# Optimization experiments

Measured on AMD Instinct MI355X. Metric: run time of the kernel, lower is better.

The kernel has to match this reference:

```python
import jax, jax.numpy as jnp
import numpy as np

G, T, D_IN, D_OUT = 8, 8192, 1024, 1024
# fixed uneven per-expert token counts summing to T (variable-size groups)
_COUNTS = np.array([512, 1536, 1024, 1024, 768, 1280, 896, 1152], dtype=np.int32)
assert _COUNTS.sum() == T


def setup_inputs() -> dict:
    key = jax.random.key(0)
    k1, k2 = jax.random.split(key)
    hidden_states = jax.random.normal(k1, (T, D_IN), dtype=jnp.float32)
    # kaiming_uniform_(a=sqrt(5)) on [G, in, out] -> bound = sqrt(3/ (fan_in)) with gain sqrt(1/3)
    bound = 1.0 / np.sqrt(D_IN)
    weight = jax.random.uniform(k2, (G, D_IN, D_OUT), dtype=jnp.float32, minval=-bound, maxval=bound)
    tokens_per_expert = jnp.asarray(_COUNTS)
    return {"hidden_states": hidden_states, "weight": weight, "tokens_per_expert": tokens_per_expert}


def reference(hidden_states, weight, tokens_per_expert):
    # grouped GEMM: token t in group g (per contiguous split by tokens_per_expert)
    # gets out[t] = hidden_states[t] @ weight[g]
    T_ = hidden_states.shape[0]
    G_ = weight.shape[0]
    offsets = jnp.cumsum(tokens_per_expert)  # [G] end offsets of each group
    expert_id = jnp.searchsorted(offsets, jnp.arange(T_), side="right")  # [T]
    out = jnp.zeros((T_, weight.shape[2]), dtype=hidden_states.dtype)
    for g in range(G_):  # small fixed expert count; masked accumulate keeps shapes static
        mask = (expert_id == g).astype(hidden_states.dtype)[:, None]
        out = out + mask * (hidden_states @ weight[g])
    return out
```

## Files before the change

kernel.cpp:

```cpp
#include <hip/hip_runtime.h>
#include <hip/hip_bf16.h>
#include <stdint.h>

typedef __attribute__((ext_vector_type(8))) short short8;
typedef __attribute__((ext_vector_type(4))) short short4s;
typedef __attribute__((ext_vector_type(4))) float f32x4;

constexpr int Tt = 8192, Kd = 1024, Nd = 1024, Gn = 8;
constexpr int BM = 128, BN = 256, BK = 64;
constexpr int NKT = Kd / BK;

static __device__ __forceinline__ short f2bf(float x) {
    __hip_bfloat16 b = __float2bfloat16(x);
    return *reinterpret_cast<short*>(&b);
}

__global__ __launch_bounds__(256)
void prep_kernel(const float* __restrict__ H, const float* __restrict__ W,
                 short* __restrict__ Hb, short* __restrict__ Wt)
{
    const int b = blockIdx.x, t = threadIdx.x;
    if (b < 2048) {
        const int g = b >> 8, r = b & 255;
        const int kb = (r >> 4) * 64, nb = (r & 15) * 64;
        const float* src = W + (size_t)g * Kd * Nd + (size_t)kb * Nd + nb;
        __shared__ float Ls[64 * 64];
#pragma unroll
        for (int i = 0; i < 4; ++i) {
            const int s = i * 256 + t;
            const int k = s >> 4, gc = s & 15;
            const f32x4 v = *(const f32x4*)(src + (size_t)k * Nd + ((gc ^ (k & 15)) << 2));
            *(f32x4*)&Ls[k * 64 + (gc << 2)] = v;
        }
        __syncthreads();
        short* dst = Wt + (size_t)g * Nd * Kd + (size_t)nb * Kd + kb;
#pragma unroll
        for (int i = 0; i < 2; ++i) {
            const int s = i * 256 + t;
            const int n = s >> 3, kc = s & 7;
            short8 v;
#pragma unroll
            for (int j = 0; j < 8; ++j) {
                const int k = kc * 8 + j;
                v[j] = f2bf(Ls[k * 64 + ((((n >> 2) ^ (k & 15)) << 2) | (n & 3))]);
            }
            *(short8*)(dst + (size_t)n * Kd + kc * 8) = v;
        }
    } else {
        const int hb = b - 2048;
#pragma unroll
        for (int i = 0; i < 8; ++i) {
            const size_t gidx = (size_t)i * 262144 + (size_t)hb * 256 + t;
            const f32x4 x = *(const f32x4*)(H + gidx * 4);
            short4s v;
#pragma unroll
            for (int j = 0; j < 4; ++j) v[j] = f2bf(x[j]);
            *(short4s*)(Hb + gidx * 4) = v;
        }
    }
}

__global__ __launch_bounds__(512, 2)
void gemm_bf16_kernel(const short* __restrict__ Hb, const short* __restrict__ Wt,
                      const int* __restrict__ counts, float* __restrict__ out)
{
    __shared__ __align__(16) short As[3][BM * BK];
    __shared__ __align__(16) short Bs[3][BN * BK];

    const int tid = threadIdx.x;
    const int bid = blockIdx.x;
    const int swz = (bid & 7) * 32 + (bid >> 3);
    const int mt = swz >> 2, nt = swz & 3;
    const int row0 = mt * BM, col0 = nt * BN;

    int g = 0;
    {
        int c = 0;
        for (int i = 0; i < Gn; ++i) { c += counts[i]; if (row0 >= c) g = i + 1; }
    }
    const short* __restrict__ Wg = Wt + (size_t)g * Nd * Kd;

    const int wid = tid >> 6, lane = tid & 63;
    const int wm = wid >> 2, wn = wid & 3;
    const int l15 = lane & 15, l4 = lane >> 4;

    f32x4 acc[4][4];
#pragma unroll
    for (int i = 0; i < 4; ++i)
#pragma unroll
        for (int j = 0; j < 4; ++j) acc[i][j] = (f32x4)0.0f;

    auto stage = [&](int kt, int buf) {
#pragma unroll
        for (int i = 0; i < 2; ++i) {
            const int q = i * 8 + wid;
            const int s = q * 64 + lane;
            const int row = s >> 3, gc = (s & 7) ^ (row & 7);
            const short* src = Hb + (size_t)(row0 + row) * Kd + kt * BK + gc * 8;
            __builtin_amdgcn_global_load_lds(
                (const __attribute__((address_space(1))) uint32_t*)src,
                (__attribute__((address_space(3))) uint32_t*)(&As[buf][q * 512]),
                16, 0, 0);
        }
#pragma unroll
        for (int i = 0; i < 4; ++i) {
            const int q = i * 8 + wid;
            const int s = q * 64 + lane;
            const int row = s >> 3, gc = (s & 7) ^ (row & 7);
            const short* src = Wg + (size_t)(col0 + row) * Kd + kt * BK + gc * 8;
            __builtin_amdgcn_global_load_lds(
                (const __attribute__((address_space(1))) uint32_t*)src,
                (__attribute__((address_space(3))) uint32_t*)(&Bs[buf][q * 512]),
                16, 0, 0);
        }
    };

    auto compute = [&](int buf) {
#pragma unroll
        for (int ks = 0; ks < 2; ++ks) {
            short8 af[4], bf[4];
#pragma unroll
            for (int mi = 0; mi < 4; ++mi) {
                const int m = wm * 64 + mi * 16 + l15;
                af[mi] = *(const short8*)&As[buf][m * 64 + (((ks * 4 + l4) ^ (m & 7)) << 3)];
            }
#pragma unroll
            for (int ni = 0; ni < 4; ++ni) {
                const int n = wn * 64 + ni * 16 + l15;
                bf[ni] = *(const short8*)&Bs[buf][n * 64 + (((ks * 4 + l4) ^ (n & 7)) << 3)];
            }
            __builtin_amdgcn_s_setprio(1);
#pragma unroll
            for (int mi = 0; mi < 4; ++mi)
#pragma unroll
                for (int ni = 0; ni < 4; ++ni)
                    acc[mi][ni] = __builtin_amdgcn_mfma_f32_16x16x32_bf16(
                        af[mi], bf[ni], acc[mi][ni], 0, 0, 0);
            __builtin_amdgcn_s_setprio(0);
        }
    };

    stage(0, 0);
    stage(1, 1);
    asm volatile("s_waitcnt vmcnt(6)" ::: "memory");
    __builtin_amdgcn_s_barrier();
    __builtin_amdgcn_sched_barrier(0);

    int b0 = 0, bs = 2;
    for (int kt = 0; kt < NKT; ++kt) {
        if (kt + 2 < NKT) stage(kt + 2, bs);
        compute(b0);
        if (kt + 1 < NKT) {
            if (kt + 2 < NKT) asm volatile("s_waitcnt vmcnt(6)" ::: "memory");
            else              asm volatile("s_waitcnt vmcnt(0)" ::: "memory");
            __builtin_amdgcn_s_barrier();
            __builtin_amdgcn_sched_barrier(0);
        }
        b0 = (b0 == 2) ? 0 : b0 + 1;
        bs = (bs == 2) ? 0 : bs + 1;
    }

#pragma unroll
    for (int mi = 0; mi < 4; ++mi) {
        const int rbase = row0 + wm * 64 + mi * 16 + l4 * 4;
#pragma unroll
        for (int ni = 0; ni < 4; ++ni) {
            const int c = col0 + wn * 64 + ni * 16 + l15;
#pragma unroll
            for (int r = 0; r < 4; ++r)
                out[(size_t)(rbase + r) * Nd + c] = acc[mi][ni][r];
        }
    }
}

__global__ __launch_bounds__(512, 2)
void gemm_f32_fallback(const float* __restrict__ H, const float* __restrict__ W,
                       const int* __restrict__ counts, float* __restrict__ out)
{
    __shared__ __align__(16) short As[2][BM * BK];
    __shared__ __align__(16) short Bs2[2][BN * BK];
    const int tid = threadIdx.x, bid = blockIdx.x;
    const int swz = (bid & 7) * 32 + (bid >> 3);
    const int mt = swz >> 2, nt = swz & 3;
    const int row0 = mt * BM, col0 = nt * BN;
    int g = 0; { int c = 0; for (int i = 0; i < Gn; ++i) { c += counts[i]; if (row0 >= c) g = i + 1; } }
    const float* __restrict__ Wg = W + (size_t)g * Kd * Nd;
    const int wid = tid >> 6, lane = tid & 63;
    const int wm = wid >> 2, wn = wid & 3;
    const int l15 = lane & 15, l4 = lane >> 4;
    const int ra = tid >> 2, ca = tid & 3;
    const int nb = tid & 255, kh = tid >> 8;
    f32x4 acc[4][4];
#pragma unroll
    for (int i = 0; i < 4; ++i)
#pragma unroll
        for (int j = 0; j < 4; ++j) acc[i][j] = (f32x4)0.0f;
    f32x4 av[4]; float bv[32];
    auto load_a = [&](int kt) {
        const float* p = H + (size_t)(row0 + ra) * Kd + kt * BK + ca * 16;
#pragma unroll
        for (int j = 0; j < 4; ++j) av[j] = *(const f32x4*)(p + j * 4);
    };
    auto load_b = [&](int kt) {
        const float* p = Wg + (size_t)(kt * BK + kh * 32) * Nd + col0 + nb;
#pragma unroll
        for (int j = 0; j < 32; ++j) bv[j] = p[(size_t)j * Nd];
    };
    auto write_a = [&](int buf) {
        short8 v0, v1;
#pragma unroll
        for (int j = 0; j < 4; ++j) {
            v0[j] = f2bf(av[0][j]); v0[4 + j] = f2bf(av[1][j]);
            v1[j] = f2bf(av[2][j]); v1[4 + j] = f2bf(av[3][j]);
        }
        const int s = ra & 7;
        *(short8*)&As[buf][ra * 64 + (((ca * 2) ^ s) << 3)] = v0;
        *(short8*)&As[buf][ra * 64 + (((ca * 2 + 1) ^ s) << 3)] = v1;
    };
    auto write_b = [&](int buf) {
        const int s = nb & 7;
#pragma unroll
        for (int c = 0; c < 4; ++c) {
            short8 v;
#pragma unroll
            for (int j = 0; j < 8; ++j) v[j] = f2bf(bv[c * 8 + j]);
            *(short8*)&Bs2[buf][nb * 64 + (((kh * 4 + c) ^ s) << 3)] = v;
        }
    };
    auto compute = [&](int buf) {
#pragma unroll
        for (int ks = 0; ks < 2; ++ks) {
            short8 af[4], bf[4];
#pragma unroll
            for (int mi = 0; mi < 4; ++mi) {
                const int m = wm * 64 + mi * 16 + l15;
                af[mi] = *(const short8*)&As[buf][m * 64 + (((ks * 4 + l4) ^ (m & 7)) << 3)];
            }
#pragma unroll
            for (int ni = 0; ni < 4; ++ni) {
                const int n = wn * 64 + ni * 16 + l15;
                bf[ni] = *(const short8*)&Bs2[buf][n * 64 + (((ks * 4 + l4) ^ (n & 7)) << 3)];
            }
#pragma unroll
            for (int mi = 0; mi < 4; ++mi)
#pragma unroll
                for (int ni = 0; ni < 4; ++ni)
                    acc[mi][ni] = __builtin_amdgcn_mfma_f32_16x16x32_bf16(
                        af[mi], bf[ni], acc[mi][ni], 0, 0, 0);
        }
    };
    load_a(0); load_b(0); write_a(0); write_b(0);
    __syncthreads();
    int buf = 0;
    for (int kt = 0; kt < NKT; ++kt) {
        const bool more = (kt + 1 < NKT);
        if (more) { load_a(kt + 1); load_b(kt + 1); }
        compute(buf);
        if (more) { write_a(buf ^ 1); write_b(buf ^ 1); }
        __syncthreads();
        buf ^= 1;
    }
#pragma unroll
    for (int mi = 0; mi < 4; ++mi) {
        const int rbase = row0 + wm * 64 + mi * 16 + l4 * 4;
#pragma unroll
        for (int ni = 0; ni < 4; ++ni) {
            const int c = col0 + wn * 64 + ni * 16 + l15;
#pragma unroll
            for (int r = 0; r < 4; ++r)
                out[(size_t)(rbase + r) * Nd + c] = acc[mi][ni][r];
        }
    }
}

extern "C" void kernel_launch(void* const* d_in, const int* in_sizes, int n_in,
                              void* d_out, int out_size, void* d_ws, size_t ws_size,
                              hipStream_t stream) {
    const float* H = (const float*)d_in[0];
    const float* W = (const float*)d_in[1];
    const int* counts = (const int*)d_in[2];
    float* out = (float*)d_out;
    const size_t need = (size_t)(Tt * Kd + Gn * Kd * Nd) * sizeof(short);
    if (ws_size >= need) {
        short* Hb = (short*)d_ws;
        short* Wt = Hb + (size_t)Tt * Kd;
        prep_kernel<<<3072, 256, 0, stream>>>(H, W, Hb, Wt);
        gemm_bf16_kernel<<<256, 512, 0, stream>>>(Hb, Wt, counts, out);
    } else {
        gemm_f32_fallback<<<256, 512, 0, stream>>>(H, W, counts, out);
    }
}
```

Before: 47.48 us.

## Split K-step into four interleaved load/read/MFMA phases with barriers

The per-K-tile work is restructured into four quadrant phases. Global-to-LDS staging of A and two halves of B is interleaved with LDS fragment reads and MFMA batches, separated by workgroup barriers, in the style of ping-pong scheduling. The goal is to overlap memory issue with matrix-core work and spread LDS traffic across the tile. The cost is many more barriers per iteration, which may add synchronisation stalls.

```diff
diff --git a/kernel.cpp b/kernel.cpp
--- a/kernel.cpp
+++ b/kernel.cpp
@@ -90,7 +90,7 @@
 #pragma unroll
         for (int j = 0; j < 4; ++j) acc[i][j] = (f32x4)0.0f;
 
-    auto stage = [&](int kt, int buf) {
+    auto stage_a = [&](int kt, int buf) {
 #pragma unroll
         for (int i = 0; i < 2; ++i) {
             const int q = i * 8 + wid;
@@ -102,9 +102,11 @@
                 (__attribute__((address_space(3))) uint32_t*)(&As[buf][q * 512]),
                 16, 0, 0);
         }
-#pragma unroll
-        for (int i = 0; i < 4; ++i) {
-            const int q = i * 8 + wid;
+    };
+    auto stage_b = [&](int kt, int buf, int half) {
+#pragma unroll
+        for (int i = 0; i < 2; ++i) {
+            const int q = (half * 2 + i) * 8 + wid;
             const int s = q * 64 + lane;
             const int row = s >> 3, gc = (s & 7) ^ (row & 7);
             const short* src = Wg + (size_t)(col0 + row) * Kd + kt * BK + gc * 8;
@@ -115,48 +117,100 @@
         }
     };
 
-    auto compute = [&](int buf) {
-#pragma unroll
-        for (int ks = 0; ks < 2; ++ks) {
-            short8 af[4], bf[4];
-#pragma unroll
-            for (int mi = 0; mi < 4; ++mi) {
-                const int m = wm * 64 + mi * 16 + l15;
-                af[mi] = *(const short8*)&As[buf][m * 64 + (((ks * 4 + l4) ^ (m & 7)) << 3)];
-            }
-#pragma unroll
-            for (int ni = 0; ni < 4; ++ni) {
-                const int n = wn * 64 + ni * 16 + l15;
-                bf[ni] = *(const short8*)&Bs[buf][n * 64 + (((ks * 4 + l4) ^ (n & 7)) << 3)];
-            }
-            __builtin_amdgcn_s_setprio(1);
-#pragma unroll
-            for (int mi = 0; mi < 4; ++mi)
-#pragma unroll
-                for (int ni = 0; ni < 4; ++ni)
-                    acc[mi][ni] = __builtin_amdgcn_mfma_f32_16x16x32_bf16(
-                        af[mi], bf[ni], acc[mi][ni], 0, 0, 0);
-            __builtin_amdgcn_s_setprio(0);
-        }
-    };
-
-    stage(0, 0);
-    stage(1, 1);
+    auto rd_a = [&](int buf, int mi, int ks) -> short8 {
+        const int m = wm * 64 + mi * 16 + l15;
+        return *(const short8*)&As[buf][m * 64 + (((ks * 4 + l4) ^ (m & 7)) << 3)];
+    };
+    auto rd_b = [&](int buf, int ni, int ks) -> short8 {
+        const int n = wn * 64 + ni * 16 + l15;
+        return *(const short8*)&Bs[buf][n * 64 + (((ks * 4 + l4) ^ (n & 7)) << 3)];
+    };
+
+    stage_a(0, 0); stage_b(0, 0, 0); stage_b(0, 0, 1);
+    stage_a(1, 1); stage_b(1, 1, 0); stage_b(1, 1, 1);
     asm volatile("s_waitcnt vmcnt(6)" ::: "memory");
     __builtin_amdgcn_s_barrier();
-    __builtin_amdgcn_sched_barrier(0);
-
-    int b0 = 0, bs = 2;
+
+    int bc = 0, bs = 2;
     for (int kt = 0; kt < NKT; ++kt) {
-        if (kt + 2 < NKT) stage(kt + 2, bs);
-        compute(b0);
-        if (kt + 1 < NKT) {
-            if (kt + 2 < NKT) asm volatile("s_waitcnt vmcnt(6)" ::: "memory");
-            else              asm volatile("s_waitcnt vmcnt(0)" ::: "memory");
-            __builtin_amdgcn_s_barrier();
-            __builtin_amdgcn_sched_barrier(0);
-        }
-        b0 = (b0 == 2) ? 0 : b0 + 1;
+        const bool pf = (kt + 2 < NKT);
+        short8 af0[2][2], af1[2][2], bf0[2][2], bf1[2][2];
+
+        if (pf) stage_a(kt + 2, bs);
+#pragma unroll
+        for (int i = 0; i < 2; ++i)
+#pragma unroll
+            for (int ks = 0; ks < 2; ++ks) { af0[i][ks] = rd_a(bc, i, ks); bf0[i][ks] = rd_b(bc, i, ks); }
+        __builtin_amdgcn_s_barrier();
+        asm volatile("s_waitcnt lgkmcnt(0)" ::: "memory");
+        __builtin_amdgcn_sched_barrier(0);
+        __builtin_amdgcn_s_setprio(1);
+#pragma unroll
+        for (int mi = 0; mi < 2; ++mi)
+#pragma unroll
+            for (int ni = 0; ni < 2; ++ni)
+#pragma unroll
+                for (int ks = 0; ks < 2; ++ks)
+                    acc[mi][ni] = __builtin_amdgcn_mfma_f32_16x16x32_bf16(
+                        af0[mi][ks], bf0[ni][ks], acc[mi][ni], 0, 0, 0);
+        __builtin_amdgcn_s_setprio(0);
+        __builtin_amdgcn_s_barrier();
+
+        if (pf) stage_b(kt + 2, bs, 0);
+#pragma unroll
+        for (int i = 0; i < 2; ++i)
+#pragma unroll
+            for (int ks = 0; ks < 2; ++ks) af1[i][ks] = rd_a(bc, 2 + i, ks);
+        __builtin_amdgcn_s_barrier();
+        asm volatile("s_waitcnt lgkmcnt(0)" ::: "memory");
+        __builtin_amdgcn_sched_barrier(0);
+        __builtin_amdgcn_s_setprio(1);
+#pragma unroll
+        for (int mi = 0; mi < 2; ++mi)
+#pragma unroll
+            for (int ni = 0; ni < 2; ++ni)
+#pragma unroll
+                for (int ks = 0; ks < 2; ++ks)
+                    acc[2 + mi][ni] = __builtin_amdgcn_mfma_f32_16x16x32_bf16(
+                        af1[mi][ks], bf0[ni][ks], acc[2 + mi][ni], 0, 0, 0);
+        __builtin_amdgcn_s_setprio(0);
+        __builtin_amdgcn_s_barrier();
+
+        if (pf) stage_b(kt + 2, bs, 1);
+#pragma unroll
+        for (int i = 0; i < 2; ++i)
+#pragma unroll
+            for (int ks = 0; ks < 2; ++ks) bf1[i][ks] = rd_b(bc, 2 + i, ks);
+        __builtin_amdgcn_s_barrier();
+        asm volatile("s_waitcnt lgkmcnt(0)" ::: "memory");
+        __builtin_amdgcn_sched_barrier(0);
+        __builtin_amdgcn_s_setprio(1);
+#pragma unroll
+        for (int mi = 0; mi < 2; ++mi)
+#pragma unroll
+            for (int ni = 0; ni < 2; ++ni)
+#pragma unroll
+                for (int ks = 0; ks < 2; ++ks)
+                    acc[2 + mi][2 + ni] = __builtin_amdgcn_mfma_f32_16x16x32_bf16(
+                        af1[mi][ks], bf1[ni][ks], acc[2 + mi][2 + ni], 0, 0, 0);
+        __builtin_amdgcn_s_setprio(0);
+        __builtin_amdgcn_s_barrier();
+
+        __builtin_amdgcn_s_setprio(1);
+#pragma unroll
+        for (int mi = 0; mi < 2; ++mi)
+#pragma unroll
+            for (int ni = 0; ni < 2; ++ni)
+#pragma unroll
+                for (int ks = 0; ks < 2; ++ks)
+                    acc[mi][2 + ni] = __builtin_amdgcn_mfma_f32_16x16x32_bf16(
+                        af0[mi][ks], bf1[ni][ks], acc[mi][2 + ni], 0, 0, 0);
+        __builtin_amdgcn_s_setprio(0);
+        if (pf)                    asm volatile("s_waitcnt vmcnt(6)" ::: "memory");
+        else if (kt + 1 < NKT)     asm volatile("s_waitcnt vmcnt(0)" ::: "memory");
+        __builtin_amdgcn_s_barrier();
+
+        bc = (bc == 2) ? 0 : bc + 1;
         bs = (bs == 2) ? 0 : bs + 1;
     }
 
```

After: 56.39 us. +18.8%, slower.

## Fuse activation bf16 conversion into GEMM A-tile loads and shrink tiles

Applied to the files above, without the earlier changes.

Drops the separate pass that converted hidden states to bf16 in workspace. The GEMM now loads fp32 activations through registers, converts them, and writes them into swizzled LDS. Block tile shrinks to 128x128 with 256 threads and 512 blocks, and the pipeline moves from a triple-buffered async global_load_lds scheme to double buffering with __syncthreads. This avoids writing and rereading the bf16 copy of H, at the cost of register-staged A loads, less latency hiding, twice the fp32 A traffic across N tiles, and removal of the setprio hints.

```diff
diff --git a/kernel.cpp b/kernel.cpp
--- a/kernel.cpp
+++ b/kernel.cpp
@@ -3,11 +3,10 @@
 #include <stdint.h>
 
 typedef __attribute__((ext_vector_type(8))) short short8;
-typedef __attribute__((ext_vector_type(4))) short short4s;
 typedef __attribute__((ext_vector_type(4))) float f32x4;
 
 constexpr int Tt = 8192, Kd = 1024, Nd = 1024, Gn = 8;
-constexpr int BM = 128, BN = 256, BK = 64;
+constexpr int BM = 128, BN = 128, BK = 64;
 constexpr int NKT = Kd / BK;
 
 static __device__ __forceinline__ short f2bf(float x) {
@@ -16,61 +15,47 @@
 }
 
 __global__ __launch_bounds__(256)
-void prep_kernel(const float* __restrict__ H, const float* __restrict__ W,
-                 short* __restrict__ Hb, short* __restrict__ Wt)
+void prep_w_kernel(const float* __restrict__ W, short* __restrict__ Wt)
 {
     const int b = blockIdx.x, t = threadIdx.x;
-    if (b < 2048) {
-        const int g = b >> 8, r = b & 255;
-        const int kb = (r >> 4) * 64, nb = (r & 15) * 64;
-        const float* src = W + (size_t)g * Kd * Nd + (size_t)kb * Nd + nb;
-        __shared__ float Ls[64 * 64];
-#pragma unroll
-        for (int i = 0; i < 4; ++i) {
-            const int s = i * 256 + t;
-            const int k = s >> 4, gc = s & 15;
-            const f32x4 v = *(const f32x4*)(src + (size_t)k * Nd + ((gc ^ (k & 15)) << 2));
-            *(f32x4*)&Ls[k * 64 + (gc << 2)] = v;
-        }
-        __syncthreads();
-        short* dst = Wt + (size_t)g * Nd * Kd + (size_t)nb * Kd + kb;
-#pragma unroll
-        for (int i = 0; i < 2; ++i) {
-            const int s = i * 256 + t;
-            const int n = s >> 3, kc = s & 7;
-            short8 v;
-#pragma unroll
-            for (int j = 0; j < 8; ++j) {
-                const int k = kc * 8 + j;
-                v[j] = f2bf(Ls[k * 64 + ((((n >> 2) ^ (k & 15)) << 2) | (n & 3))]);
-            }
-            *(short8*)(dst + (size_t)n * Kd + kc * 8) = v;
-        }
-    } else {
-        const int hb = b - 2048;
-#pragma unroll
-        for (int i = 0; i < 8; ++i) {
-            const size_t gidx = (size_t)i * 262144 + (size_t)hb * 256 + t;
-            const f32x4 x = *(const f32x4*)(H + gidx * 4);
-            short4s v;
-#pragma unroll
-            for (int j = 0; j < 4; ++j) v[j] = f2bf(x[j]);
-            *(short4s*)(Hb + gidx * 4) = v;
-        }
-    }
-}
-
-__global__ __launch_bounds__(512, 2)
-void gemm_bf16_kernel(const short* __restrict__ Hb, const short* __restrict__ Wt,
-                      const int* __restrict__ counts, float* __restrict__ out)
+    const int g = b >> 8, r = b & 255;
+    const int kb = (r >> 4) * 64, nb = (r & 15) * 64;
+    const float* src = W + (size_t)g * Kd * Nd + (size_t)kb * Nd + nb;
+    __shared__ float Ls[64 * 64];
+#pragma unroll
+    for (int i = 0; i < 4; ++i) {
+        const int s = i * 256 + t;
+        const int k = s >> 4, gc = s & 15;
+        const f32x4 v = *(const f32x4*)(src + (size_t)k * Nd + ((gc ^ (k & 15)) << 2));
+        *(f32x4*)&Ls[k * 64 + (gc << 2)] = v;
+    }
+    __syncthreads();
+    short* dst = Wt + (size_t)g * Nd * Kd + (size_t)nb * Kd + kb;
+#pragma unroll
+    for (int i = 0; i < 2; ++i) {
+        const int s = i * 256 + t;
+        const int n = s >> 3, kc = s & 7;
+        short8 v;
+#pragma unroll
+        for (int j = 0; j < 8; ++j) {
+            const int k = kc * 8 + j;
+            v[j] = f2bf(Ls[k * 64 + ((((n >> 2) ^ (k & 15)) << 2) | (n & 3))]);
+        }
+        *(short8*)(dst + (size_t)n * Kd + kc * 8) = v;
+    }
+}
+
+__global__ __launch_bounds__(256, 2)
+void gemm_kernel(const float* __restrict__ H, const short* __restrict__ Wt,
+                 const int* __restrict__ counts, float* __restrict__ out)
 {
-    __shared__ __align__(16) short As[3][BM * BK];
-    __shared__ __align__(16) short Bs[3][BN * BK];
+    __shared__ __align__(16) short As[2][BM * BK];
+    __shared__ __align__(16) short Bs[2][BN * BK];
 
     const int tid = threadIdx.x;
     const int bid = blockIdx.x;
-    const int swz = (bid & 7) * 32 + (bid >> 3);
-    const int mt = swz >> 2, nt = swz & 3;
+    const int wg = (bid & 7) * 64 + (bid >> 3);
+    const int mt = wg >> 3, nt = wg & 7;
     const int row0 = mt * BM, col0 = nt * BN;
 
     int g = 0;
@@ -81,7 +66,7 @@
     const short* __restrict__ Wg = Wt + (size_t)g * Nd * Kd;
 
     const int wid = tid >> 6, lane = tid & 63;
-    const int wm = wid >> 2, wn = wid & 3;
+    const int wm = wid >> 1, wn = wid & 1;
     const int l15 = lane & 15, l4 = lane >> 4;
 
     f32x4 acc[4][4];
@@ -90,24 +75,31 @@
 #pragma unroll
         for (int j = 0; j < 4; ++j) acc[i][j] = (f32x4)0.0f;
 
-    auto stage = [&](int kt, int buf) {
-#pragma unroll
-        for (int i = 0; i < 2; ++i) {
-            const int q = i * 8 + wid;
+    const int ra = tid >> 1, kh = tid & 1;
+    f32x4 av[8];
+
+    auto load_a = [&](int kt) {
+        const float* p = H + (size_t)(row0 + ra) * Kd + kt * BK + kh * 32;
+#pragma unroll
+        for (int j = 0; j < 8; ++j) av[j] = *(const f32x4*)(p + j * 4);
+    };
+    auto write_a = [&](int buf) {
+        const int s = ra & 7;
+#pragma unroll
+        for (int c = 0; c < 4; ++c) {
+            short8 v;
+#pragma unroll
+            for (int j = 0; j < 4; ++j) { v[j] = f2bf(av[2 * c][j]); v[4 + j] = f2bf(av[2 * c + 1][j]); }
+            *(short8*)&As[buf][ra * 64 + (((kh * 4 + c) ^ s) << 3)] = v;
+        }
+    };
+    auto stage_b = [&](int kt, int buf) {
+#pragma unroll
+        for (int i = 0; i < 4; ++i) {
+            const int q = i * 4 + wid;
             const int s = q * 64 + lane;
-            const int row = s >> 3, gc = (s & 7) ^ (row & 7);
-            const short* src = Hb + (size_t)(row0 + row) * Kd + kt * BK + gc * 8;
-            __builtin_amdgcn_global_load_lds(
-                (const __attribute__((address_space(1))) uint32_t*)src,
-                (__attribute__((address_space(3))) uint32_t*)(&As[buf][q * 512]),
-                16, 0, 0);
-        }
-#pragma unroll
-        for (int i = 0; i < 4; ++i) {
-            const int q = i * 8 + wid;
-            const int s = q * 64 + lane;
-            const int row = s >> 3, gc = (s & 7) ^ (row & 7);
-            const short* src = Wg + (size_t)(col0 + row) * Kd + kt * BK + gc * 8;
+            const int rowb = s >> 3, gc = (s & 7) ^ (rowb & 7);
+            const short* src = Wg + (size_t)(col0 + rowb) * Kd + kt * BK + gc * 8;
             __builtin_amdgcn_global_load_lds(
                 (const __attribute__((address_space(1))) uint32_t*)src,
                 (__attribute__((address_space(3))) uint32_t*)(&Bs[buf][q * 512]),
@@ -129,35 +121,28 @@
                 const int n = wn * 64 + ni * 16 + l15;
                 bf[ni] = *(const short8*)&Bs[buf][n * 64 + (((ks * 4 + l4) ^ (n & 7)) << 3)];
             }
-            __builtin_amdgcn_s_setprio(1);
 #pragma unroll
             for (int mi = 0; mi < 4; ++mi)
 #pragma unroll
                 for (int ni = 0; ni < 4; ++ni)
                     acc[mi][ni] = __builtin_amdgcn_mfma_f32_16x16x32_bf16(
                         af[mi], bf[ni], acc[mi][ni], 0, 0, 0);
-            __builtin_amdgcn_s_setprio(0);
-        }
-    };
-
-    stage(0, 0);
-    stage(1, 1);
-    asm volatile("s_waitcnt vmcnt(6)" ::: "memory");
-    __builtin_amdgcn_s_barrier();
-    __builtin_amdgcn_sched_barrier(0);
-
-    int b0 = 0, bs = 2;
+        }
+    };
+
+    load_a(0);
+    stage_b(0, 0);
+    write_a(0);
+    __syncthreads();
+
+    int buf = 0;
     for (int kt = 0; kt < NKT; ++kt) {
-        if (kt + 2 < NKT) stage(kt + 2, bs);
-        compute(b0);
-        if (kt + 1 < NKT) {
-            if (kt + 2 < NKT) asm volatile("s_waitcnt vmcnt(6)" ::: "memory");
-            else              asm volatile("s_waitcnt vmcnt(0)" ::: "memory");
-            __builtin_amdgcn_s_barrier();
-            __builtin_amdgcn_sched_barrier(0);
-        }
-        b0 = (b0 == 2) ? 0 : b0 + 1;
-        bs = (bs == 2) ? 0 : bs + 1;
+        const bool more = (kt + 1 < NKT);
+        if (more) { stage_b(kt + 1, buf ^ 1); load_a(kt + 1); }
+        compute(buf);
+        if (more) write_a(buf ^ 1);
+        __syncthreads();
+        buf ^= 1;
     }
 
 #pragma unroll
@@ -177,12 +162,13 @@
 void gemm_f32_fallback(const float* __restrict__ H, const float* __restrict__ W,
                        const int* __restrict__ counts, float* __restrict__ out)
 {
+    constexpr int FBN = 256;
     __shared__ __align__(16) short As[2][BM * BK];
-    __shared__ __align__(16) short Bs2[2][BN * BK];
+    __shared__ __align__(16) short Bs2[2][FBN * BK];
     const int tid = threadIdx.x, bid = blockIdx.x;
     const int swz = (bid & 7) * 32 + (bid >> 3);
     const int mt = swz >> 2, nt = swz & 3;
-    const int row0 = mt * BM, col0 = nt * BN;
+    const int row0 = mt * BM, col0 = nt * FBN;
     int g = 0; { int c = 0; for (int i = 0; i < Gn; ++i) { c += counts[i]; if (row0 >= c) g = i + 1; } }
     const float* __restrict__ Wg = W + (size_t)g * Kd * Nd;
     const int wid = tid >> 6, lane = tid & 63;
@@ -280,12 +266,11 @@
     const float* W = (const float*)d_in[1];
     const int* counts = (const int*)d_in[2];
     float* out = (float*)d_out;
-    const size_t need = (size_t)(Tt * Kd + Gn * Kd * Nd) * sizeof(short);
+    const size_t need = (size_t)Gn * Kd * Nd * sizeof(short);
     if (ws_size >= need) {
-        short* Hb = (short*)d_ws;
-        short* Wt = Hb + (size_t)Tt * Kd;
-        prep_kernel<<<3072, 256, 0, stream>>>(H, W, Hb, Wt);
-        gemm_bf16_kernel<<<256, 512, 0, stream>>>(Hb, Wt, counts, out);
+        short* Wt = (short*)d_ws;
+        prep_w_kernel<<<2048, 256, 0, stream>>>(W, Wt);
+        gemm_kernel<<<512, 256, 0, stream>>>(H, Wt, counts, out);
     } else {
         gemm_f32_fallback<<<256, 512, 0, stream>>>(H, W, counts, out);
     }
```

Result: slower. 58.45 us (+23.1%).
